# Performance work log

Hardware: AMD Instinct MI355X
Metric: run time of the kernel (lower is better)

The kernel has to match this reference:

```python
import jax, jax.numpy as jnp
import numpy as np


def _squash(x, eps=1e-8):
    # squash along last (feature) dim: v = s * ||s||^2 / (1+||s||^2) / ||s||
    n2 = jnp.sum(x * x, axis=-1, keepdims=True)
    return x * (n2 / (1.0 + n2)) / jnp.sqrt(n2 + eps)


def setup_inputs() -> dict:
    key = jax.random.key(0)
    k1, k2 = jax.random.split(key)
    B, N_IN, N_CAPS, N_FEAT = 16, 2048, 64, 16
    inputs = jax.random.normal(k1, (B, N_IN, N_CAPS, N_FEAT), dtype=jnp.float32)
    bias = jax.random.normal(k2, (N_CAPS, N_FEAT), dtype=jnp.float32) * 0.02
    return {"inputs": inputs, "bias": bias, "num_routing": 3}


def reference(inputs, bias, num_routing):
    # inputs: [B, n_in, n_caps, n_feat]; bias: [n_caps, n_feat]
    priors = jnp.zeros_like(inputs)
    outputs = None
    for i in range(num_routing):
        agreements = jax.nn.softmax(priors, axis=-2)            # over n_caps
        outputs = jnp.sum(inputs * agreements, axis=-3, keepdims=True)  # [B,1,n_caps,n_feat]
        outputs = _squash(outputs + bias)
        if i < num_routing - 1:
            priors = priors + jnp.sum(inputs * outputs, axis=-1, keepdims=True)
    return outputs[:, 0]  # [B, n_caps, n_feat]
```

## Files before the change

kernel.cpp:

```cpp
#include <hip/hip_runtime.h>
#include <hip/hip_fp16.h>
#include <math.h>

#define BB 16
#define NIN 2048
#define NC 64
#define NF 16
#define BLOCKS_PER_B 128
#define I_PER_BLOCK (NIN / BLOCKS_PER_B)
#define I_PER_WAVE (I_PER_BLOCK / 4)
#define NPART (BB * BLOCKS_PER_B)

__device__ __forceinline__ float dot4(float4 a, float4 b) {
    return a.x * b.x + a.y * b.y + a.z * b.z + a.w * b.w;
}

__device__ __forceinline__ float4 half4_to_float4(uint2 u) {
    __half2 h0 = *reinterpret_cast<__half2*>(&u.x);
    __half2 h1 = *reinterpret_cast<__half2*>(&u.y);
    float2 f0 = __half22float2(h0);
    float2 f1 = __half22float2(h1);
    return make_float4(f0.x, f0.y, f1.x, f1.y);
}

__global__ __launch_bounds__(256) void pass_mean(const float* __restrict__ in,
                                                 float* __restrict__ part,
                                                 uint2* __restrict__ cp) {
    const int b = blockIdx.x >> 7;
    const int blk = blockIdx.x & 127;
    const int lane = threadIdx.x & 63;
    const int wave = threadIdx.x >> 6;
    const float4* in4 = (const float4*)in;

    float4 acc[4];
#pragma unroll
    for (int k = 0; k < 4; ++k) acc[k] = make_float4(0.f, 0.f, 0.f, 0.f);

    const size_t base =
        ((size_t)b * NIN + (size_t)blk * I_PER_BLOCK + (size_t)wave * I_PER_WAVE) * 256;
#pragma unroll
    for (int t = 0; t < I_PER_WAVE; ++t) {
        const float4* p = in4 + base + (size_t)t * 256;
        uint2* q = cp + base + (size_t)t * 256;
#pragma unroll
        for (int k = 0; k < 4; ++k) {
            float4 v = p[lane + (k << 6)];
            acc[k].x += v.x; acc[k].y += v.y; acc[k].z += v.z; acc[k].w += v.w;
            __half2 h0 = __float22half2_rn(make_float2(v.x, v.y));
            __half2 h1 = __float22half2_rn(make_float2(v.z, v.w));
            uint2 u;
            u.x = *reinterpret_cast<unsigned*>(&h0);
            u.y = *reinterpret_cast<unsigned*>(&h1);
            q[lane + (k << 6)] = u;
        }
    }

    __shared__ float4 red[4 * 256];
#pragma unroll
    for (int k = 0; k < 4; ++k) red[wave * 256 + lane + (k << 6)] = acc[k];
    __syncthreads();

    const int t = threadIdx.x;
    float4 s0 = red[t], s1 = red[256 + t], s2 = red[512 + t], s3 = red[768 + t];
    float4* g = (float4*)(part + (size_t)blockIdx.x * 1024) + t;
    *g = make_float4(s0.x + s1.x + s2.x + s3.x, s0.y + s1.y + s2.y + s3.y,
                     s0.z + s1.z + s2.z + s3.z, s0.w + s1.w + s2.w + s3.w);
}

__global__ __launch_bounds__(256) void pass_route(const uint2* __restrict__ in2,
                                                  const float* __restrict__ wv,
                                                  float* __restrict__ part) {
    const int b = blockIdx.x >> 7;
    const int blk = blockIdx.x & 127;
    const int lane = threadIdx.x & 63;
    const int wave = threadIdx.x >> 6;
    const float4* wv4 = (const float4*)wv + (size_t)b * 256;

    float4 ow[4];
#pragma unroll
    for (int k = 0; k < 4; ++k) ow[k] = wv4[lane + (k << 6)];

    float4 acc[4];
#pragma unroll
    for (int k = 0; k < 4; ++k) acc[k] = make_float4(0.f, 0.f, 0.f, 0.f);

    const size_t base =
        ((size_t)b * NIN + (size_t)blk * I_PER_BLOCK + (size_t)wave * I_PER_WAVE) * 256;
    for (int t = 0; t < I_PER_WAVE; ++t) {
        const uint2* p = in2 + base + (size_t)t * 256;
        float4 v[4];
        float d[4];
#pragma unroll
        for (int k = 0; k < 4; ++k) v[k] = half4_to_float4(p[lane + (k << 6)]);
#pragma unroll
        for (int k = 0; k < 4; ++k) {
            d[k] = dot4(v[k], ow[k]);
            d[k] += __shfl_xor(d[k], 1);
            d[k] += __shfl_xor(d[k], 2);
        }
        float e[4];
        float ssum = 0.f;
#pragma unroll
        for (int k = 0; k < 4; ++k) {
            e[k] = __expf(d[k]);
            ssum += e[k];
        }
        ssum += __shfl_xor(ssum, 4);
        ssum += __shfl_xor(ssum, 8);
        ssum += __shfl_xor(ssum, 16);
        ssum += __shfl_xor(ssum, 32);
        const float inv = 1.0f / ssum;
#pragma unroll
        for (int k = 0; k < 4; ++k) {
            const float a = e[k] * inv;
            acc[k].x += a * v[k].x;
            acc[k].y += a * v[k].y;
            acc[k].z += a * v[k].z;
            acc[k].w += a * v[k].w;
        }
    }

    __shared__ float4 red[4 * 256];
#pragma unroll
    for (int k = 0; k < 4; ++k) red[wave * 256 + lane + (k << 6)] = acc[k];
    __syncthreads();

    const int t = threadIdx.x;
    float4 s0 = red[t], s1 = red[256 + t], s2 = red[512 + t], s3 = red[768 + t];
    float4* g = (float4*)(part + (size_t)blockIdx.x * 1024) + t;
    *g = make_float4(s0.x + s1.x + s2.x + s3.x, s0.y + s1.y + s2.y + s3.y,
                     s0.z + s1.z + s2.z + s3.z, s0.w + s1.w + s2.w + s3.w);
}

__global__ __launch_bounds__(256) void reduce_squash(const float* __restrict__ part,
                                                     const float* __restrict__ bias,
                                                     const float* __restrict__ prev,
                                                     float* __restrict__ dst,
                                                     float scale) {
    const int b = blockIdx.x >> 6;
    const int c = blockIdx.x & 63;
    const int tid = threadIdx.x;
    const int f = tid & 15;
    const int pc = tid >> 4;

    const float* p = part + (size_t)(b * BLOCKS_PER_B) * 1024 + c * NF + f;
    float sum = 0.f;
#pragma unroll
    for (int j = 0; j < 8; ++j) sum += p[(size_t)(pc + 16 * j) * 1024];

    __shared__ float red[256];
    red[tid] = sum;
    __syncthreads();
    if (tid < 128) red[tid] += red[tid + 128];
    __syncthreads();
    if (tid < 64) red[tid] += red[tid + 64];
    __syncthreads();
    if (tid < 32) red[tid] += red[tid + 32];
    __syncthreads();
    if (tid < 16) {
        float s = (red[tid] + red[tid + 16]) * scale + bias[c * NF + f];
        float n2 = s * s;
        n2 += __shfl_xor(n2, 1);
        n2 += __shfl_xor(n2, 2);
        n2 += __shfl_xor(n2, 4);
        n2 += __shfl_xor(n2, 8);
        const float sc = n2 / (1.0f + n2) / sqrtf(n2 + 1e-8f);
        float o = s * sc;
        const size_t oi = (size_t)b * 1024 + c * NF + f;
        if (prev) o += prev[oi];
        dst[oi] = o;
    }
}

extern "C" void kernel_launch(void* const* d_in, const int* in_sizes, int n_in,
                              void* d_out, int out_size, void* d_ws, size_t ws_size,
                              hipStream_t stream) {
    const float* in = (const float*)d_in[0];
    const float* bias = (const float*)d_in[1];

    float* ws = (float*)d_ws;
    float* part = ws;
    float* out0 = ws + (size_t)NPART * 1024;
    float* osum = out0 + 16384;
    uint2* cp = (uint2*)(osum + 16384);

    dim3 grid(NPART), blk(256);
    pass_mean<<<grid, blk, 0, stream>>>(in, part, cp);
    reduce_squash<<<1024, 256, 0, stream>>>(part, bias, nullptr, out0, 1.0f / 64.0f);
    pass_route<<<grid, blk, 0, stream>>>(cp, out0, part);
    reduce_squash<<<1024, 256, 0, stream>>>(part, bias, out0, osum, 1.0f);
    pass_route<<<grid, blk, 0, stream>>>(cp, osum, part);
    reduce_squash<<<1024, 256, 0, stream>>>(part, bias, nullptr, (float*)d_out, 1.0f);
}
```

Baseline: 80.88 us.

## Remap route pass to one capsule per lane with 16-byte loads and full preload

Each lane of pass_route now owns one whole capsule (16 features) and reads it with two 16-byte loads, instead of spreading a capsule over four lanes with 8-byte loads. The per-capsule dot product becomes a plain in-register sum with no cross-lane shuffles, and only the softmax denominator still needs a wave-wide reduction. All four rows per wave are preloaded before any compute to expose memory-level parallelism. The block reduction moves to a padded LDS layout to fit the new mapping. The preload and wider accumulators raise register use.

```diff
diff --git a/kernel.cpp b/kernel.cpp
--- a/kernel.cpp
+++ b/kernel.cpp
@@ -21,6 +21,14 @@
     float2 f0 = __half22float2(h0);
     float2 f1 = __half22float2(h1);
     return make_float4(f0.x, f0.y, f1.x, f1.y);
+}
+
+__device__ __forceinline__ float4 unpack4(unsigned a, unsigned b) {
+    __half2 ha = *reinterpret_cast<__half2*>(&a);
+    __half2 hb = *reinterpret_cast<__half2*>(&b);
+    float2 fa = __half22float2(ha);
+    float2 fb = __half22float2(hb);
+    return make_float4(fa.x, fa.y, fb.x, fb.y);
 }
 
 __global__ __launch_bounds__(256) void pass_mean(const float* __restrict__ in,
@@ -67,7 +75,7 @@
                      s0.z + s1.z + s2.z + s3.z, s0.w + s1.w + s2.w + s3.w);
 }
 
-__global__ __launch_bounds__(256) void pass_route(const uint2* __restrict__ in2,
+__global__ __launch_bounds__(256) void pass_route(const uint4* __restrict__ cp4,
                                                   const float* __restrict__ wv,
                                                   float* __restrict__ part) {
     const int b = blockIdx.x >> 7;
@@ -76,60 +84,66 @@
     const int wave = threadIdx.x >> 6;
     const float4* wv4 = (const float4*)wv + (size_t)b * 256;
 
-    float4 ow[4];
-#pragma unroll
-    for (int k = 0; k < 4; ++k) ow[k] = wv4[lane + (k << 6)];
-
-    float4 acc[4];
-#pragma unroll
-    for (int k = 0; k < 4; ++k) acc[k] = make_float4(0.f, 0.f, 0.f, 0.f);
-
-    const size_t base =
-        ((size_t)b * NIN + (size_t)blk * I_PER_BLOCK + (size_t)wave * I_PER_WAVE) * 256;
-    for (int t = 0; t < I_PER_WAVE; ++t) {
-        const uint2* p = in2 + base + (size_t)t * 256;
-        float4 v[4];
-        float d[4];
-#pragma unroll
-        for (int k = 0; k < 4; ++k) v[k] = half4_to_float4(p[lane + (k << 6)]);
-#pragma unroll
-        for (int k = 0; k < 4; ++k) {
-            d[k] = dot4(v[k], ow[k]);
-            d[k] += __shfl_xor(d[k], 1);
-            d[k] += __shfl_xor(d[k], 2);
-        }
-        float e[4];
-        float ssum = 0.f;
-#pragma unroll
-        for (int k = 0; k < 4; ++k) {
-            e[k] = __expf(d[k]);
-            ssum += e[k];
-        }
-        ssum += __shfl_xor(ssum, 4);
-        ssum += __shfl_xor(ssum, 8);
-        ssum += __shfl_xor(ssum, 16);
-        ssum += __shfl_xor(ssum, 32);
-        const float inv = 1.0f / ssum;
-#pragma unroll
-        for (int k = 0; k < 4; ++k) {
-            const float a = e[k] * inv;
-            acc[k].x += a * v[k].x;
-            acc[k].y += a * v[k].y;
-            acc[k].z += a * v[k].z;
-            acc[k].w += a * v[k].w;
-        }
-    }
-
-    __shared__ float4 red[4 * 256];
-#pragma unroll
-    for (int k = 0; k < 4; ++k) red[wave * 256 + lane + (k << 6)] = acc[k];
+    const float4 w0 = wv4[4 * lane];
+    const float4 w1 = wv4[4 * lane + 1];
+    const float4 w2 = wv4[4 * lane + 2];
+    const float4 w3 = wv4[4 * lane + 3];
+
+    float4 acc0 = make_float4(0.f, 0.f, 0.f, 0.f);
+    float4 acc1 = acc0, acc2 = acc0, acc3 = acc0;
+
+    const size_t i0 = (size_t)b * NIN + (size_t)blk * I_PER_BLOCK + (size_t)wave * I_PER_WAVE;
+
+    uint4 u[I_PER_WAVE][2];
+#pragma unroll
+    for (int r = 0; r < I_PER_WAVE; ++r) {
+        u[r][0] = cp4[(i0 + r) * 128 + 2 * lane];
+        u[r][1] = cp4[(i0 + r) * 128 + 2 * lane + 1];
+    }
+
+#pragma unroll
+    for (int r = 0; r < I_PER_WAVE; ++r) {
+        float4 v0 = unpack4(u[r][0].x, u[r][0].y);
+        float4 v1 = unpack4(u[r][0].z, u[r][0].w);
+        float4 v2 = unpack4(u[r][1].x, u[r][1].y);
+        float4 v3 = unpack4(u[r][1].z, u[r][1].w);
+        float d = dot4(v0, w0) + dot4(v1, w1) + dot4(v2, w2) + dot4(v3, w3);
+        float e = __expf(d);
+        float ss = e;
+        ss += __shfl_xor(ss, 1);
+        ss += __shfl_xor(ss, 2);
+        ss += __shfl_xor(ss, 4);
+        ss += __shfl_xor(ss, 8);
+        ss += __shfl_xor(ss, 16);
+        ss += __shfl_xor(ss, 32);
+        const float a = e / ss;
+        acc0.x += a * v0.x; acc0.y += a * v0.y; acc0.z += a * v0.z; acc0.w += a * v0.w;
+        acc1.x += a * v1.x; acc1.y += a * v1.y; acc1.z += a * v1.z; acc1.w += a * v1.w;
+        acc2.x += a * v2.x; acc2.y += a * v2.y; acc2.z += a * v2.z; acc2.w += a * v2.w;
+        acc3.x += a * v3.x; acc3.y += a * v3.y; acc3.z += a * v3.z; acc3.w += a * v3.w;
+    }
+
+    __shared__ float lds[4 * 64 * 20];
+    {
+        float* myl = &lds[(wave * 64 + lane) * 20];
+        *(float4*)(myl + 0) = acc0;
+        *(float4*)(myl + 4) = acc1;
+        *(float4*)(myl + 8) = acc2;
+        *(float4*)(myl + 12) = acc3;
+    }
     __syncthreads();
 
     const int t = threadIdx.x;
-    float4 s0 = red[t], s1 = red[256 + t], s2 = red[512 + t], s3 = red[768 + t];
-    float4* g = (float4*)(part + (size_t)blockIdx.x * 1024) + t;
-    *g = make_float4(s0.x + s1.x + s2.x + s3.x, s0.y + s1.y + s2.y + s3.y,
-                     s0.z + s1.z + s2.z + s3.z, s0.w + s1.w + s2.w + s3.w);
+    const int c = t >> 2;
+    const int j = t & 3;
+    float4 s = *(const float4*)&lds[(0 * 64 + c) * 20 + 4 * j];
+#pragma unroll
+    for (int w = 1; w < 4; ++w) {
+        float4 r = *(const float4*)&lds[(w * 64 + c) * 20 + 4 * j];
+        s.x += r.x; s.y += r.y; s.z += r.z; s.w += r.w;
+    }
+    float4* g = (float4*)(part + (size_t)blockIdx.x * 1024) + (c * 4 + j);
+    *g = s;
 }
 
 __global__ __launch_bounds__(256) void reduce_squash(const float* __restrict__ part,
@@ -187,8 +201,8 @@
     dim3 grid(NPART), blk(256);
     pass_mean<<<grid, blk, 0, stream>>>(in, part, cp);
     reduce_squash<<<1024, 256, 0, stream>>>(part, bias, nullptr, out0, 1.0f / 64.0f);
-    pass_route<<<grid, blk, 0, stream>>>(cp, out0, part);
+    pass_route<<<grid, blk, 0, stream>>>((const uint4*)cp, out0, part);
     reduce_squash<<<1024, 256, 0, stream>>>(part, bias, out0, osum, 1.0f);
-    pass_route<<<grid, blk, 0, stream>>>(cp, osum, part);
+    pass_route<<<grid, blk, 0, stream>>>((const uint4*)cp, osum, part);
     reduce_squash<<<1024, 256, 0, stream>>>(part, bias, nullptr, (float*)d_out, 1.0f);
 }
```

Result: no change. 80.75 us (-0.2%).
